# Kernel tuning notes

Hardware: AMD Instinct MI355X
Metric: run time of the kernel (lower is better)

Reference implementation:

```python
import jax, jax.numpy as jnp
import numpy as np
from jax import lax

N, D, H = 4096, 256, 4


def setup_inputs() -> dict:
    key = jax.random.key(0)
    ks = jax.random.split(key, 6)
    x = jax.random.normal(ks[0], (1, 1, N, D), dtype=jnp.float32)
    adj = jax.random.randint(ks[1], (N, N), 0, 2, dtype=jnp.int32)
    conv_w = jax.random.normal(ks[2], (1, 1, 1, 1), dtype=jnp.float32)
    conv_b = jax.random.normal(ks[3], (1,), dtype=jnp.float32)
    # xavier_uniform on (H, 2D, 1) with gain 1.414
    limit = 1.414 * np.sqrt(6.0 / (2 * D + 1))
    a = jax.random.uniform(ks[4], (H, 2 * D, 1), minval=-limit, maxval=limit, dtype=jnp.float32)
    bias = jnp.zeros((D,), dtype=jnp.float32)
    return {"x": x, "adj": adj, "conv_w": conv_w, "conv_b": conv_b, "a": a, "bias": bias}


def reference(x, adj, conv_w, conv_b, a, bias):
    # 1x1 conv (NCHW / OIHW), preserves spatial dims
    h = lax.conv_general_dilated(x, conv_w, (1, 1), 'VALID',
                                 dimension_numbers=('NCHW', 'OIHW', 'NCHW'))
    h = h + conv_b[None, :, None, None]
    h = h[0, 0]                      # [N, D]
    d = h.shape[1]
    a1 = a[:, :d, 0]                 # [H, D]
    a2 = a[:, d:, 0]                 # [H, D]
    Wh1 = h @ a1.T                   # [N, H]
    Wh2 = h @ a2.T                   # [N, H]
    # e[k, i, j] = elu(Wh1[i, k] + Wh2[j, k])
    e = jax.nn.elu(Wh1.T[:, :, None] + Wh2.T[:, None, :])   # [H, N, N]
    att = jnp.where((adj > 0)[None, :, :], e, jnp.float32(-9e15))
    att = jax.nn.softmax(att, axis=-1)
    # dropout is inactive in eval mode (self.training=False)
    h_pass = jnp.einsum('hij,jd->hid', att, h).mean(axis=0)  # [N, D]
    out = jax.nn.elu(0.5 * h_pass + 0.5 * h)
    norm = jnp.maximum(jnp.linalg.norm(out, axis=1, keepdims=True), 1e-12)
    out = out / norm
    return out + bias
```

## Files before the change

### kernel.cpp

```cpp
#include <hip/hip_runtime.h>
#include <math.h>

#define NN 4096
#define DD 256
#define HH 4
#define SPLIT 8
#define BM 64
#define BK 64
#define STR 72

typedef short short8 __attribute__((ext_vector_type(8)));
typedef float float4v __attribute__((ext_vector_type(4)));

__device__ __forceinline__ unsigned short f2bf(float f) {
  unsigned u = __float_as_uint(f);
  u += 0x7FFF + ((u >> 16) & 1);
  return (unsigned short)(u >> 16);
}
__device__ __forceinline__ float bf2f(unsigned short s) {
  return __uint_as_float(((unsigned)s) << 16);
}

__global__ void k_zero(float* __restrict__ hp) {
  int idx = blockIdx.x * 256 + threadIdx.x;
  ((float4*)hp)[idx] = make_float4(0.f, 0.f, 0.f, 0.f);
}

__global__ void k_prep(const float* __restrict__ x, const float* __restrict__ cwp,
                       const float* __restrict__ cbp, unsigned short* __restrict__ hbfT) {
  __shared__ unsigned short t[64 * 257];
  const int tid = threadIdx.x;
  const int j0 = blockIdx.x * 64;
  const float cw = cwp[0], cb = cbp[0];
  for (int jj = 0; jj < 64; jj++) {
    float v = x[(size_t)(j0 + jj) * DD + tid] * cw + cb;
    t[jj * 257 + tid] = f2bf(v);
  }
  __syncthreads();
  const int jj = tid & 63, dq = tid >> 6;
  for (int k = 0; k < 64; k++) {
    const int d = k * 4 + dq;
    hbfT[(size_t)d * NN + j0 + jj] = t[jj * 257 + d];
  }
}

__global__ void k_scores(const float* __restrict__ x, const float* __restrict__ a,
                         const float* __restrict__ cwp, const float* __restrict__ cbp,
                         float* __restrict__ s1, float* __restrict__ s2) {
  const int lane = threadIdx.x & 63;
  const int wave = threadIdx.x >> 6;
  const int node = blockIdx.x * 4 + wave;
  const float cw = cwp[0], cb = cbp[0];
  const float4 xv = *(const float4*)(x + (size_t)node * DD + lane * 4);
  float4 hv;
  hv.x = xv.x * cw + cb; hv.y = xv.y * cw + cb;
  hv.z = xv.z * cw + cb; hv.w = xv.w * cw + cb;
  float p1[HH], p2[HH];
#pragma unroll
  for (int h = 0; h < HH; h++) {
    const float4 a1 = *(const float4*)(a + h * 512 + lane * 4);
    const float4 a2 = *(const float4*)(a + h * 512 + 256 + lane * 4);
    p1[h] = hv.x * a1.x + hv.y * a1.y + hv.z * a1.z + hv.w * a1.w;
    p2[h] = hv.x * a2.x + hv.y * a2.y + hv.z * a2.z + hv.w * a2.w;
  }
#pragma unroll
  for (int off = 32; off; off >>= 1) {
#pragma unroll
    for (int h = 0; h < HH; h++) {
      p1[h] += __shfl_xor(p1[h], off);
      p2[h] += __shfl_xor(p2[h], off);
    }
  }
  if (lane == 0) {
#pragma unroll
    for (int h = 0; h < HH; h++) {
      s1[h * NN + node] = p1[h];
      s2[h * NN + node] = p2[h];
    }
  }
}

__global__ void k_maxs2(const float* __restrict__ s2, float* __restrict__ M) {
  const int h = blockIdx.x;
  float m = -1e30f;
  for (int j = threadIdx.x; j < NN; j += 256) m = fmaxf(m, s2[h * NN + j]);
#pragma unroll
  for (int off = 32; off; off >>= 1) m = fmaxf(m, __shfl_xor(m, off));
  __shared__ float red[4];
  const int lane = threadIdx.x & 63, wave = threadIdx.x >> 6;
  if (lane == 0) red[wave] = m;
  __syncthreads();
  if (threadIdx.x == 0)
    M[h] = fmaxf(fmaxf(red[0], red[1]), fmaxf(red[2], red[3]));
}

__global__ __launch_bounds__(256) void k_zw(
    const int* __restrict__ adj, const float* __restrict__ s1g,
    const float* __restrict__ s2g, const float* __restrict__ Mb,
    unsigned short* __restrict__ Wm) {
  __shared__ unsigned short sP[HH][NN];
  __shared__ float red[4][HH];
  __shared__ float sZi[HH];

  const int i = blockIdx.x;
  const int tid = threadIdx.x;
  float s1v[HH], Bv[HH], z[HH];
#pragma unroll
  for (int h = 0; h < HH; h++) {
    s1v[h] = s1g[h * NN + i];
    const float t = s1v[h] + Mb[h];
    Bv[h] = t > 0.f ? t : __expf(t) - 1.f;
    z[h] = 0.f;
  }
  const int4* arow = (const int4*)(adj + (size_t)i * NN);
#pragma unroll
  for (int j4 = tid; j4 < NN / 4; j4 += 256) {
    const int4 av = arow[j4];
#pragma unroll
    for (int h = 0; h < HH; h++) {
      const float4 sv = *(const float4*)(s2g + h * NN + j4 * 4);
      float t, e, p0, p1, p2, p3;
      t = s1v[h] + sv.x; e = t > 0.f ? t : __expf(t) - 1.f;
      p0 = av.x > 0 ? __expf(e - Bv[h]) : 0.f;
      t = s1v[h] + sv.y; e = t > 0.f ? t : __expf(t) - 1.f;
      p1 = av.y > 0 ? __expf(e - Bv[h]) : 0.f;
      t = s1v[h] + sv.z; e = t > 0.f ? t : __expf(t) - 1.f;
      p2 = av.z > 0 ? __expf(e - Bv[h]) : 0.f;
      t = s1v[h] + sv.w; e = t > 0.f ? t : __expf(t) - 1.f;
      p3 = av.w > 0 ? __expf(e - Bv[h]) : 0.f;
      z[h] += (p0 + p1) + (p2 + p3);
      ushort4 pk;
      pk.x = f2bf(p0); pk.y = f2bf(p1); pk.z = f2bf(p2); pk.w = f2bf(p3);
      *(ushort4*)&sP[h][j4 * 4] = pk;
    }
  }
#pragma unroll
  for (int h = 0; h < HH; h++) {
#pragma unroll
    for (int off = 32; off; off >>= 1) z[h] += __shfl_xor(z[h], off);
  }
  const int lane = tid & 63, wave = tid >> 6;
  if (lane == 0) {
#pragma unroll
    for (int h = 0; h < HH; h++) red[wave][h] = z[h];
  }
  __syncthreads();
  if (tid < HH) {
    const float zt = red[0][tid] + red[1][tid] + red[2][tid] + red[3][tid];
    sZi[tid] = zt > 0.f ? 0.25f / zt : 0.f;
  }
  __syncthreads();
  float Zi[HH];
#pragma unroll
  for (int h = 0; h < HH; h++) Zi[h] = sZi[h];

  unsigned short* wrow = Wm + (size_t)i * NN;
#pragma unroll
  for (int j4 = tid; j4 < NN / 4; j4 += 256) {
    float w0 = 0.f, w1 = 0.f, w2 = 0.f, w3 = 0.f;
#pragma unroll
    for (int h = 0; h < HH; h++) {
      const ushort4 pk = *(const ushort4*)&sP[h][j4 * 4];
      w0 += bf2f(pk.x) * Zi[h];
      w1 += bf2f(pk.y) * Zi[h];
      w2 += bf2f(pk.z) * Zi[h];
      w3 += bf2f(pk.w) * Zi[h];
    }
    ushort4 wk;
    wk.x = f2bf(w0); wk.y = f2bf(w1); wk.z = f2bf(w2); wk.w = f2bf(w3);
    *(ushort4*)&wrow[j4 * 4] = wk;
  }
}

__global__ __launch_bounds__(256) void k_gemm(
    const unsigned short* __restrict__ Wm, const unsigned short* __restrict__ hbfT,
    float* __restrict__ hpOut) {
  __shared__ __align__(16) unsigned short sW[BM * STR];
  __shared__ __align__(16) unsigned short sH[DD * STR];

  const int tid = threadIdx.x;
  const int w = tid >> 6, lane = tid & 63;
  const int m16 = lane & 15, q = lane >> 4;
  const int rb = blockIdx.x >> 3, sp = blockIdx.x & 7;
  const int i0 = rb * BM;
  const int jlo = sp * (NN / SPLIT);
  const int r0 = tid >> 3;
  const int c0 = tid & 7;

  float4v acc[4][4];
#pragma unroll
  for (int a = 0; a < 4; a++)
#pragma unroll
    for (int b = 0; b < 4; b++) acc[a][b] = (float4v)0.f;

  for (int kt = 0; kt < (NN / SPLIT) / BK; kt++) {
    const int j0 = jlo + kt * BK;
    __syncthreads();
#pragma unroll
    for (int r = 0; r < 2; r++) {
      const int row = r * 32 + r0;
      *(float4*)(sW + row * STR + c0 * 8) =
          *(const float4*)(Wm + (size_t)(i0 + row) * NN + j0 + c0 * 8);
    }
#pragma unroll
    for (int r = 0; r < 8; r++) {
      const int d = r * 32 + r0;
      *(float4*)(sH + d * STR + c0 * 8) =
          *(const float4*)(hbfT + (size_t)d * NN + j0 + c0 * 8);
    }
    __syncthreads();
#pragma unroll
    for (int ks = 0; ks < 2; ks++) {
      const int kb = ks * 32 + q * 8;
      short8 aF[4], bF[4];
#pragma unroll
      for (int it = 0; it < 4; it++)
        aF[it] = *(const short8*)(sW + (it * 16 + m16) * STR + kb);
#pragma unroll
      for (int dt = 0; dt < 4; dt++)
        bF[dt] = *(const short8*)(sH + (w * 64 + dt * 16 + m16) * STR + kb);
#pragma unroll
      for (int it = 0; it < 4; it++)
#pragma unroll
        for (int dt = 0; dt < 4; dt++)
          acc[it][dt] = __builtin_amdgcn_mfma_f32_16x16x32_bf16(aF[it], bF[dt], acc[it][dt], 0, 0, 0);
    }
  }

  float* base = hpOut + (size_t)sp * NN * DD;
#pragma unroll
  for (int it = 0; it < 4; it++)
#pragma unroll
    for (int dt = 0; dt < 4; dt++) {
      const int d = w * 64 + dt * 16 + m16;
#pragma unroll
      for (int rg = 0; rg < 4; rg++) {
        const int i = i0 + it * 16 + q * 4 + rg;
        base[(size_t)i * DD + d] = acc[it][dt][rg];
      }
    }
}

__global__ void k_z(const int* __restrict__ adj, const float* __restrict__ s1,
                    const float* __restrict__ s2, const float* __restrict__ Mb,
                    float* __restrict__ Bb, float* __restrict__ Zb) {
  const int i = blockIdx.x;
  float s1v[HH], Bv[HH], z[HH];
#pragma unroll
  for (int h = 0; h < HH; h++) {
    s1v[h] = s1[h * NN + i];
    const float t = s1v[h] + Mb[h];
    Bv[h] = t > 0.f ? t : __expf(t) - 1.f;
    z[h] = 0.f;
  }
  const int4* arow = (const int4*)(adj + (size_t)i * NN);
  for (int j4 = threadIdx.x; j4 < NN / 4; j4 += 256) {
    const int4 av = arow[j4];
#pragma unroll
    for (int h = 0; h < HH; h++) {
      const float4 sv = *(const float4*)(s2 + h * NN + j4 * 4);
      float t, e;
      t = s1v[h] + sv.x; e = t > 0.f ? t : __expf(t) - 1.f;
      z[h] += av.x > 0 ? __expf(e - Bv[h]) : 0.f;
      t = s1v[h] + sv.y; e = t > 0.f ? t : __expf(t) - 1.f;
      z[h] += av.y > 0 ? __expf(e - Bv[h]) : 0.f;
      t = s1v[h] + sv.z; e = t > 0.f ? t : __expf(t) - 1.f;
      z[h] += av.z > 0 ? __expf(e - Bv[h]) : 0.f;
      t = s1v[h] + sv.w; e = t > 0.f ? t : __expf(t) - 1.f;
      z[h] += av.w > 0 ? __expf(e - Bv[h]) : 0.f;
    }
  }
#pragma unroll
  for (int h = 0; h < HH; h++) {
#pragma unroll
    for (int off = 32; off; off >>= 1) z[h] += __shfl_xor(z[h], off);
  }
  __shared__ float red[4][HH];
  const int lane = threadIdx.x & 63, wave = threadIdx.x >> 6;
  if (lane == 0) {
#pragma unroll
    for (int h = 0; h < HH; h++) red[wave][h] = z[h];
  }
  __syncthreads();
  if (threadIdx.x == 0) {
#pragma unroll
    for (int h = 0; h < HH; h++) {
      Zb[h * NN + i] = red[0][h] + red[1][h] + red[2][h] + red[3][h];
      Bb[h * NN + i] = Bv[h];
    }
  }
}

__global__ __launch_bounds__(256) void k_agg_fused(
    const int* __restrict__ adj, const unsigned short* __restrict__ hbfT,
    const float* __restrict__ s1, const float* __restrict__ s2,
    const float* __restrict__ Bb, const float* __restrict__ Zb,
    float* __restrict__ hpOut, int useSplit) {
  __shared__ unsigned short sW[BM * STR];
  __shared__ unsigned short sH[DD * STR];
  __shared__ float sS1[HH][BM], sB[HH][BM], sZi[HH][BM], ss2[HH][BK];

  const int tid = threadIdx.x;
  const int w = tid >> 6, lane = tid & 63;
  const int m16 = lane & 15, q = lane >> 4;
  const int rb = blockIdx.x >> 3, sp = blockIdx.x & 7;
  const int i0 = rb * BM;
  const int jlo = sp * (NN / SPLIT);

  {
    const float zv = Zb[w * NN + i0 + lane];
    sS1[w][lane] = s1[w * NN + i0 + lane];
    sB[w][lane] = Bb[w * NN + i0 + lane];
    sZi[w][lane] = zv > 0.f ? 0.25f / zv : 0.f;
  }

  float4v acc[4][4];
#pragma unroll
  for (int a = 0; a < 4; a++)
#pragma unroll
    for (int b = 0; b < 4; b++) acc[a][b] = (float4v)0.f;

  for (int kt = 0; kt < (NN / SPLIT) / BK; kt++) {
    const int j0 = jlo + kt * BK;
    __syncthreads();
    ss2[w][lane] = s2[w * NN + j0 + lane];
    {
      const int dbase = tid >> 3, part = tid & 7;
#pragma unroll
      for (int r = 0; r < 8; r++) {
        const int d = dbase + r * 32;
        const float4 v = *(const float4*)(hbfT + (size_t)d * NN + j0 + part * 8);
        *(float4*)(sH + d * STR + part * 8) = v;
      }
    }
    __syncthreads();
    {
      const int jj = lane;
#pragma unroll
      for (int r = 0; r < 16; r++) {
        const int ii = r * 4 + w;
        const int av = adj[(size_t)(i0 + ii) * NN + j0 + jj];
        float wsum = 0.f;
#pragma unroll
        for (int h = 0; h < HH; h++) {
          const float tv = sS1[h][ii] + ss2[h][jj];
          const float e = tv > 0.f ? tv : __expf(tv) - 1.f;
          wsum += __expf(e - sB[h][ii]) * sZi[h][ii];
        }
        sW[ii * STR + jj] = av > 0 ? f2bf(wsum) : (unsigned short)0;
      }
    }
    __syncthreads();
#pragma unroll
    for (int ks = 0; ks < 2; ks++) {
      const int kb = ks * 32 + q * 8;
      short8 aF[4], bF[4];
#pragma unroll
      for (int it = 0; it < 4; it++)
        aF[it] = *(const short8*)(sW + (it * 16 + m16) * STR + kb);
#pragma unroll
      for (int dt = 0; dt < 4; dt++)
        bF[dt] = *(const short8*)(sH + (w * 64 + dt * 16 + m16) * STR + kb);
#pragma unroll
      for (int it = 0; it < 4; it++)
#pragma unroll
        for (int dt = 0; dt < 4; dt++)
          acc[it][dt] = __builtin_amdgcn_mfma_f32_16x16x32_bf16(aF[it], bF[dt], acc[it][dt], 0, 0, 0);
    }
  }

  if (useSplit) {
    float* base = hpOut + (size_t)sp * NN * DD;
#pragma unroll
    for (int it = 0; it < 4; it++)
#pragma unroll
      for (int dt = 0; dt < 4; dt++) {
        const int d = w * 64 + dt * 16 + m16;
#pragma unroll
        for (int rg = 0; rg < 4; rg++) {
          const int i = i0 + it * 16 + q * 4 + rg;
          base[(size_t)i * DD + d] = acc[it][dt][rg];
        }
      }
  } else {
#pragma unroll
    for (int it = 0; it < 4; it++)
#pragma unroll
      for (int dt = 0; dt < 4; dt++) {
        const int d = w * 64 + dt * 16 + m16;
#pragma unroll
        for (int rg = 0; rg < 4; rg++) {
          const int i = i0 + it * 16 + q * 4 + rg;
          atomicAdd(&hpOut[(size_t)i * DD + d], acc[it][dt][rg]);
        }
      }
  }
}

__global__ void k_epi(const float* __restrict__ hp, int nsplit,
                      const float* __restrict__ x, const float* __restrict__ cwp,
                      const float* __restrict__ cbp, const float* __restrict__ bias,
                      float* __restrict__ out) {
  const int lane = threadIdx.x & 63, wave = threadIdx.x >> 6;
  const int i = blockIdx.x * 4 + wave;
  const float cw = cwp[0], cb = cbp[0];
  float o[4];
  float ss = 0.f;
#pragma unroll
  for (int k = 0; k < 4; k++) {
    const int d = lane + 64 * k;
    float pv = 0.f;
    for (int s = 0; s < nsplit; s++)
      pv += hp[(size_t)s * NN * DD + (size_t)i * DD + d];
    const float hv = x[(size_t)i * DD + d] * cw + cb;
    float v = 0.5f * pv + 0.5f * hv;
    v = v > 0.f ? v : expm1f(v);
    o[k] = v;
    ss += v * v;
  }
#pragma unroll
  for (int off = 32; off; off >>= 1) ss += __shfl_xor(ss, off);
  const float inv = 1.f / fmaxf(sqrtf(ss), 1e-12f);
#pragma unroll
  for (int k = 0; k < 4; k++) {
    const int d = lane + 64 * k;
    out[(size_t)i * DD + d] = o[k] * inv + bias[d];
  }
}

extern "C" void kernel_launch(void* const* d_in, const int* in_sizes, int n_in,
                              void* d_out, int out_size, void* d_ws, size_t ws_size,
                              hipStream_t stream) {
  const float* x = (const float*)d_in[0];
  const int* adj = (const int*)d_in[1];
  const float* cw = (const float*)d_in[2];
  const float* cb = (const float*)d_in[3];
  const float* a = (const float*)d_in[4];
  const float* bias = (const float*)d_in[5];
  float* out = (float*)d_out;
  float* ws = (float*)d_ws;

  const size_t newNeed = (size_t)(16384 * 2 + 256 + 524288 + 8388608 + 8388608) * 4;

  if (ws_size >= newNeed) {
    float* s1 = ws;
    float* s2 = ws + 16384;
    float* Mb = ws + 32768;
    unsigned short* hbfT = (unsigned short*)(ws + 33024);
    unsigned short* Wm = (unsigned short*)(ws + 33024 + 524288);
    float* hp = ws + 33024 + 524288 + 8388608;

    hipLaunchKernelGGL(k_prep, dim3(64), dim3(256), 0, stream, x, cw, cb, hbfT);
    hipLaunchKernelGGL(k_scores, dim3(1024), dim3(256), 0, stream, x, a, cw, cb, s1, s2);
    hipLaunchKernelGGL(k_maxs2, dim3(HH), dim3(256), 0, stream, s2, Mb);
    hipLaunchKernelGGL(k_zw, dim3(NN), dim3(256), 0, stream, adj, s1, s2, Mb, Wm);
    hipLaunchKernelGGL(k_gemm, dim3((NN / BM) * SPLIT), dim3(256), 0, stream, Wm, hbfT, hp);
    hipLaunchKernelGGL(k_epi, dim3(1024), dim3(256), 0, stream, hp, SPLIT, x, cw, cb, bias, out);
  } else {
    float* s1 = ws;
    float* s2 = ws + 16384;
    float* Zb = ws + 32768;
    float* Bb = ws + 49152;
    float* Mb = ws + 65536;
    unsigned short* hbfT = (unsigned short*)(ws + 65792);
    float* hp = ws + 65792 + 524288;

    const size_t needSplit = (size_t)(65792 + 524288 + SPLIT * NN * DD) * 4;
    const int useSplit = (ws_size >= needSplit) ? 1 : 0;
    const int nsplit = useSplit ? SPLIT : 1;

    if (!useSplit) hipLaunchKernelGGL(k_zero, dim3(1024), dim3(256), 0, stream, hp);
    hipLaunchKernelGGL(k_prep, dim3(64), dim3(256), 0, stream, x, cw, cb, hbfT);
    hipLaunchKernelGGL(k_scores, dim3(1024), dim3(256), 0, stream, x, a, cw, cb, s1, s2);
    hipLaunchKernelGGL(k_maxs2, dim3(HH), dim3(256), 0, stream, s2, Mb);
    hipLaunchKernelGGL(k_z, dim3(NN), dim3(256), 0, stream, adj, s1, s2, Mb, Bb, Zb);
    hipLaunchKernelGGL(k_agg_fused, dim3((NN / BM) * SPLIT), dim3(256), 0, stream,
                       adj, hbfT, s1, s2, Bb, Zb, hp, useSplit);
    hipLaunchKernelGGL(k_epi, dim3(1024), dim3(256), 0, stream, hp, nsplit, x, cw, cb, bias, out);
  }
}
```

Measured before the change: 178.0 us.

## Factor exp of scores, packed bf16 stores, direct-load GEMM, tiled prep

Attention weights are rewritten as exp(elu(s1+s2)-B) using a precomputed exp(s2), so the positive branch needs one multiply and only the negative branch calls exp. Pairs of bf16 values are packed with a byte permute instead of being handled as separate shorts. The GEMM drops LDS staging and loads MFMA fragments straight from global memory, relying on the cache for reuse. The prep transpose is retiled into 256 smaller blocks. The exp(s2) rewrite can overflow for large scores, and the fallback path passes Bb as the s2e output, which k_z then overwrites.

```diff
diff --git a/kernel.cpp b/kernel.cpp
--- a/kernel.cpp
+++ b/kernel.cpp
@@ -17,8 +17,10 @@
   u += 0x7FFF + ((u >> 16) & 1);
   return (unsigned short)(u >> 16);
 }
-__device__ __forceinline__ float bf2f(unsigned short s) {
-  return __uint_as_float(((unsigned)s) << 16);
+__device__ __forceinline__ unsigned int f2bf_pk(float a, float b) {
+  unsigned ua = __float_as_uint(a); ua += 0x7FFF + ((ua >> 16) & 1);
+  unsigned ub = __float_as_uint(b); ub += 0x7FFF + ((ub >> 16) & 1);
+  return __builtin_amdgcn_perm(ub, ua, 0x07060302);
 }
 
 __global__ void k_zero(float* __restrict__ hp) {
@@ -26,27 +28,38 @@
   ((float4*)hp)[idx] = make_float4(0.f, 0.f, 0.f, 0.f);
 }
 
-__global__ void k_prep(const float* __restrict__ x, const float* __restrict__ cwp,
-                       const float* __restrict__ cbp, unsigned short* __restrict__ hbfT) {
-  __shared__ unsigned short t[64 * 257];
+__global__ __launch_bounds__(256) void k_prep(const float* __restrict__ x,
+                                              const float* __restrict__ cwp,
+                                              const float* __restrict__ cbp,
+                                              unsigned short* __restrict__ hbfT) {
+  __shared__ float t[64][65];
+  const int j0 = (blockIdx.x & 63) * 64;
+  const int d0 = (blockIdx.x >> 6) * 64;
   const int tid = threadIdx.x;
-  const int j0 = blockIdx.x * 64;
   const float cw = cwp[0], cb = cbp[0];
-  for (int jj = 0; jj < 64; jj++) {
-    float v = x[(size_t)(j0 + jj) * DD + tid] * cw + cb;
-    t[jj * 257 + tid] = f2bf(v);
+  const int r = tid >> 4, c4 = tid & 15;
+#pragma unroll
+  for (int p = 0; p < 4; p++) {
+    const int jj = p * 16 + r;
+    const float4 v = *(const float4*)(x + (size_t)(j0 + jj) * DD + d0 + c4 * 4);
+    t[jj][c4 * 4 + 0] = v.x * cw + cb;
+    t[jj][c4 * 4 + 1] = v.y * cw + cb;
+    t[jj][c4 * 4 + 2] = v.z * cw + cb;
+    t[jj][c4 * 4 + 3] = v.w * cw + cb;
   }
   __syncthreads();
   const int jj = tid & 63, dq = tid >> 6;
-  for (int k = 0; k < 64; k++) {
-    const int d = k * 4 + dq;
-    hbfT[(size_t)d * NN + j0 + jj] = t[jj * 257 + d];
+#pragma unroll
+  for (int k = 0; k < 16; k++) {
+    const int dd = k * 4 + dq;
+    hbfT[(size_t)(d0 + dd) * NN + j0 + jj] = f2bf(t[jj][dd]);
   }
 }
 
 __global__ void k_scores(const float* __restrict__ x, const float* __restrict__ a,
                          const float* __restrict__ cwp, const float* __restrict__ cbp,
-                         float* __restrict__ s1, float* __restrict__ s2) {
+                         float* __restrict__ s1, float* __restrict__ s2,
+                         float* __restrict__ s2e) {
   const int lane = threadIdx.x & 63;
   const int wave = threadIdx.x >> 6;
   const int node = blockIdx.x * 4 + wave;
@@ -76,6 +89,7 @@
     for (int h = 0; h < HH; h++) {
       s1[h * NN + node] = p1[h];
       s2[h * NN + node] = p2[h];
+      s2e[h * NN + node] = __expf(p2[h]);
     }
   }
 }
@@ -96,42 +110,42 @@
 
 __global__ __launch_bounds__(256) void k_zw(
     const int* __restrict__ adj, const float* __restrict__ s1g,
-    const float* __restrict__ s2g, const float* __restrict__ Mb,
+    const float* __restrict__ s2e, const float* __restrict__ Mb,
     unsigned short* __restrict__ Wm) {
-  __shared__ unsigned short sP[HH][NN];
+  __shared__ unsigned int sP[HH][NN / 2];
   __shared__ float red[4][HH];
   __shared__ float sZi[HH];
 
   const int i = blockIdx.x;
   const int tid = threadIdx.x;
-  float s1v[HH], Bv[HH], z[HH];
+  float Rp[HH], RpRB[HH], Cc[HH], z[HH];
 #pragma unroll
   for (int h = 0; h < HH; h++) {
-    s1v[h] = s1g[h * NN + i];
-    const float t = s1v[h] + Mb[h];
-    Bv[h] = t > 0.f ? t : __expf(t) - 1.f;
+    const float s1v = s1g[h * NN + i];
+    const float t = s1v + Mb[h];
+    const float B = t > 0.f ? t : __expf(t) - 1.f;
+    Rp[h] = __expf(s1v);
+    RpRB[h] = __expf(s1v - B);
+    Cc[h] = __expf(-1.f - B);
     z[h] = 0.f;
   }
   const int4* arow = (const int4*)(adj + (size_t)i * NN);
-#pragma unroll
   for (int j4 = tid; j4 < NN / 4; j4 += 256) {
     const int4 av = arow[j4];
-#pragma unroll
-    for (int h = 0; h < HH; h++) {
-      const float4 sv = *(const float4*)(s2g + h * NN + j4 * 4);
-      float t, e, p0, p1, p2, p3;
-      t = s1v[h] + sv.x; e = t > 0.f ? t : __expf(t) - 1.f;
-      p0 = av.x > 0 ? __expf(e - Bv[h]) : 0.f;
-      t = s1v[h] + sv.y; e = t > 0.f ? t : __expf(t) - 1.f;
-      p1 = av.y > 0 ? __expf(e - Bv[h]) : 0.f;
-      t = s1v[h] + sv.z; e = t > 0.f ? t : __expf(t) - 1.f;
-      p2 = av.z > 0 ? __expf(e - Bv[h]) : 0.f;
-      t = s1v[h] + sv.w; e = t > 0.f ? t : __expf(t) - 1.f;
-      p3 = av.w > 0 ? __expf(e - Bv[h]) : 0.f;
+    const bool m0 = av.x > 0, m1 = av.y > 0, m2 = av.z > 0, m3 = av.w > 0;
+#pragma unroll
+    for (int h = 0; h < HH; h++) {
+      const float4 E = *(const float4*)(s2e + h * NN + j4 * 4);
+      float u, p0, p1, p2, p3;
+      u = Rp[h] * E.x; p0 = u > 1.f ? RpRB[h] * E.x : Cc[h] * __expf(u);
+      u = Rp[h] * E.y; p1 = u > 1.f ? RpRB[h] * E.y : Cc[h] * __expf(u);
+      u = Rp[h] * E.z; p2 = u > 1.f ? RpRB[h] * E.z : Cc[h] * __expf(u);
+      u = Rp[h] * E.w; p3 = u > 1.f ? RpRB[h] * E.w : Cc[h] * __expf(u);
+      p0 = m0 ? p0 : 0.f; p1 = m1 ? p1 : 0.f;
+      p2 = m2 ? p2 : 0.f; p3 = m3 ? p3 : 0.f;
       z[h] += (p0 + p1) + (p2 + p3);
-      ushort4 pk;
-      pk.x = f2bf(p0); pk.y = f2bf(p1); pk.z = f2bf(p2); pk.w = f2bf(p3);
-      *(ushort4*)&sP[h][j4 * 4] = pk;
+      sP[h][j4 * 2] = f2bf_pk(p0, p1);
+      sP[h][j4 * 2 + 1] = f2bf_pk(p2, p3);
     }
   }
 #pragma unroll
@@ -154,38 +168,35 @@
 #pragma unroll
   for (int h = 0; h < HH; h++) Zi[h] = sZi[h];
 
-  unsigned short* wrow = Wm + (size_t)i * NN;
-#pragma unroll
+  unsigned int* wrow = (unsigned int*)(Wm + (size_t)i * NN);
   for (int j4 = tid; j4 < NN / 4; j4 += 256) {
     float w0 = 0.f, w1 = 0.f, w2 = 0.f, w3 = 0.f;
 #pragma unroll
     for (int h = 0; h < HH; h++) {
-      const ushort4 pk = *(const ushort4*)&sP[h][j4 * 4];
-      w0 += bf2f(pk.x) * Zi[h];
-      w1 += bf2f(pk.y) * Zi[h];
-      w2 += bf2f(pk.z) * Zi[h];
-      w3 += bf2f(pk.w) * Zi[h];
-    }
-    ushort4 wk;
-    wk.x = f2bf(w0); wk.y = f2bf(w1); wk.z = f2bf(w2); wk.w = f2bf(w3);
-    *(ushort4*)&wrow[j4 * 4] = wk;
+      const unsigned int pa = sP[h][j4 * 2];
+      const unsigned int pb = sP[h][j4 * 2 + 1];
+      w0 += __uint_as_float(pa << 16) * Zi[h];
+      w1 += __uint_as_float(pa & 0xffff0000u) * Zi[h];
+      w2 += __uint_as_float(pb << 16) * Zi[h];
+      w3 += __uint_as_float(pb & 0xffff0000u) * Zi[h];
+    }
+    wrow[j4 * 2] = f2bf_pk(w0, w1);
+    wrow[j4 * 2 + 1] = f2bf_pk(w2, w3);
   }
 }
 
 __global__ __launch_bounds__(256) void k_gemm(
     const unsigned short* __restrict__ Wm, const unsigned short* __restrict__ hbfT,
     float* __restrict__ hpOut) {
-  __shared__ __align__(16) unsigned short sW[BM * STR];
-  __shared__ __align__(16) unsigned short sH[DD * STR];
-
   const int tid = threadIdx.x;
   const int w = tid >> 6, lane = tid & 63;
   const int m16 = lane & 15, q = lane >> 4;
   const int rb = blockIdx.x >> 3, sp = blockIdx.x & 7;
   const int i0 = rb * BM;
   const int jlo = sp * (NN / SPLIT);
-  const int r0 = tid >> 3;
-  const int c0 = tid & 7;
+
+  const unsigned short* Ab = Wm + (size_t)(i0 + m16) * NN + jlo + q * 8;
+  const unsigned short* Bb = hbfT + (size_t)(w * 64 + m16) * NN + jlo + q * 8;
 
   float4v acc[4][4];
 #pragma unroll
@@ -193,38 +204,26 @@
 #pragma unroll
     for (int b = 0; b < 4; b++) acc[a][b] = (float4v)0.f;
 
+#pragma unroll 2
   for (int kt = 0; kt < (NN / SPLIT) / BK; kt++) {
-    const int j0 = jlo + kt * BK;
-    __syncthreads();
-#pragma unroll
-    for (int r = 0; r < 2; r++) {
-      const int row = r * 32 + r0;
-      *(float4*)(sW + row * STR + c0 * 8) =
-          *(const float4*)(Wm + (size_t)(i0 + row) * NN + j0 + c0 * 8);
-    }
-#pragma unroll
-    for (int r = 0; r < 8; r++) {
-      const int d = r * 32 + r0;
-      *(float4*)(sH + d * STR + c0 * 8) =
-          *(const float4*)(hbfT + (size_t)d * NN + j0 + c0 * 8);
-    }
-    __syncthreads();
-#pragma unroll
-    for (int ks = 0; ks < 2; ks++) {
-      const int kb = ks * 32 + q * 8;
-      short8 aF[4], bF[4];
+    short8 aF[2][4], bF[2][4];
+#pragma unroll
+    for (int ks = 0; ks < 2; ks++)
 #pragma unroll
       for (int it = 0; it < 4; it++)
-        aF[it] = *(const short8*)(sW + (it * 16 + m16) * STR + kb);
+        aF[ks][it] = *(const short8*)(Ab + (size_t)it * 16 * NN + kt * BK + ks * 32);
+#pragma unroll
+    for (int ks = 0; ks < 2; ks++)
 #pragma unroll
       for (int dt = 0; dt < 4; dt++)
-        bF[dt] = *(const short8*)(sH + (w * 64 + dt * 16 + m16) * STR + kb);
+        bF[ks][dt] = *(const short8*)(Bb + (size_t)dt * 16 * NN + kt * BK + ks * 32);
+#pragma unroll
+    for (int ks = 0; ks < 2; ks++)
 #pragma unroll
       for (int it = 0; it < 4; it++)
 #pragma unroll
         for (int dt = 0; dt < 4; dt++)
-          acc[it][dt] = __builtin_amdgcn_mfma_f32_16x16x32_bf16(aF[it], bF[dt], acc[it][dt], 0, 0, 0);
-    }
+          acc[it][dt] = __builtin_amdgcn_mfma_f32_16x16x32_bf16(aF[ks][it], bF[ks][dt], acc[it][dt], 0, 0, 0);
   }
 
   float* base = hpOut + (size_t)sp * NN * DD;
@@ -440,20 +439,21 @@
   float* out = (float*)d_out;
   float* ws = (float*)d_ws;
 
-  const size_t newNeed = (size_t)(16384 * 2 + 256 + 524288 + 8388608 + 8388608) * 4;
+  const size_t newNeed = (size_t)(16384 * 3 + 256 + 524288 + 8388608 + 8388608) * 4;
 
   if (ws_size >= newNeed) {
     float* s1 = ws;
     float* s2 = ws + 16384;
-    float* Mb = ws + 32768;
-    unsigned short* hbfT = (unsigned short*)(ws + 33024);
-    unsigned short* Wm = (unsigned short*)(ws + 33024 + 524288);
-    float* hp = ws + 33024 + 524288 + 8388608;
-
-    hipLaunchKernelGGL(k_prep, dim3(64), dim3(256), 0, stream, x, cw, cb, hbfT);
-    hipLaunchKernelGGL(k_scores, dim3(1024), dim3(256), 0, stream, x, a, cw, cb, s1, s2);
+    float* s2e = ws + 32768;
+    float* Mb = ws + 49152;
+    unsigned short* hbfT = (unsigned short*)(ws + 49408);
+    unsigned short* Wm = (unsigned short*)(ws + 49408 + 524288);
+    float* hp = ws + 49408 + 524288 + 8388608;
+
+    hipLaunchKernelGGL(k_prep, dim3(256), dim3(256), 0, stream, x, cw, cb, hbfT);
+    hipLaunchKernelGGL(k_scores, dim3(1024), dim3(256), 0, stream, x, a, cw, cb, s1, s2, s2e);
     hipLaunchKernelGGL(k_maxs2, dim3(HH), dim3(256), 0, stream, s2, Mb);
-    hipLaunchKernelGGL(k_zw, dim3(NN), dim3(256), 0, stream, adj, s1, s2, Mb, Wm);
+    hipLaunchKernelGGL(k_zw, dim3(NN), dim3(256), 0, stream, adj, s1, s2e, Mb, Wm);
     hipLaunchKernelGGL(k_gemm, dim3((NN / BM) * SPLIT), dim3(256), 0, stream, Wm, hbfT, hp);
     hipLaunchKernelGGL(k_epi, dim3(1024), dim3(256), 0, stream, hp, SPLIT, x, cw, cb, bias, out);
   } else {
@@ -470,8 +470,8 @@
     const int nsplit = useSplit ? SPLIT : 1;
 
     if (!useSplit) hipLaunchKernelGGL(k_zero, dim3(1024), dim3(256), 0, stream, hp);
-    hipLaunchKernelGGL(k_prep, dim3(64), dim3(256), 0, stream, x, cw, cb, hbfT);
-    hipLaunchKernelGGL(k_scores, dim3(1024), dim3(256), 0, stream, x, a, cw, cb, s1, s2);
+    hipLaunchKernelGGL(k_prep, dim3(256), dim3(256), 0, stream, x, cw, cb, hbfT);
+    hipLaunchKernelGGL(k_scores, dim3(1024), dim3(256), 0, stream, x, a, cw, cb, s1, s2, Bb);
     hipLaunchKernelGGL(k_maxs2, dim3(HH), dim3(256), 0, stream, s2, Mb);
     hipLaunchKernelGGL(k_z, dim3(NN), dim3(256), 0, stream, adj, s1, s2, Mb, Bb, Zb);
     hipLaunchKernelGGL(k_agg_fused, dim3((NN / BM) * SPLIT), dim3(256), 0, stream,
```

Result: slower. 186.1 us (+4.5%).
